# Kernel tuning notes

Measured on AMD Instinct MI355X. Metric: run time of the kernel, lower is better.

Reference implementation:

```python
import jax, jax.numpy as jnp
import numpy as np

N, E = 100_000, 1_600_000
NDIM_IN, EDIM, F, H, C = 64, 32, 32, 3, 10  # F=ndim_out per head, H=num_heads


def _edge_softmax(scores, dst, n):
    # softmax over incoming edges grouped by destination node (DGL edge_softmax)
    m = jax.ops.segment_max(scores, dst, num_segments=n)          # [N,H]
    ex = jnp.exp(scores - m[dst])                                  # [E,H]
    s = jax.ops.segment_sum(ex, dst, num_segments=n)               # [N,H]
    return ex / s[dst]


def _egat_conv(nf, ef, src, dst, W, We, al, ar, ae, b, n):
    # DGL EdgeGATConv: edge features modulate attention logits only
    h, f = al.shape
    ft = (nf @ W).reshape(-1, h, f)      # [N,H,F]
    fe = (ef @ We).reshape(-1, h, f)     # [E,H,F]
    el = (ft * al).sum(-1)               # [N,H]
    er = (ft * ar).sum(-1)               # [N,H]
    ee = (fe * ae).sum(-1)               # [E,H]
    e = jax.nn.leaky_relu(el[src] + er[dst] + ee, 0.2)             # [E,H]
    a = _edge_softmax(e, dst, n)                                   # [E,H]
    rst = jax.ops.segment_sum(ft[src] * a[:, :, None], dst, num_segments=n)
    return rst + b.reshape(1, h, f)


def setup_inputs() -> dict:
    key = jax.random.key(0)
    ks = jax.random.split(key, 16)
    s = lambda k, shp, fan: (jax.random.normal(k, shp, jnp.float32) / np.sqrt(fan).astype(np.float32))
    d = {}
    d["nfeats"] = jax.random.normal(ks[0], (N, 1, NDIM_IN), jnp.float32)
    d["efeats"] = jax.random.normal(ks[1], (E, 1, EDIM), jnp.float32)
    d["src"] = jax.random.randint(ks[2], (E,), 0, N, jnp.int32)
    d["dst"] = jax.random.randint(ks[3], (E,), 0, N, jnp.int32)
    # conv1 params
    d["W1"] = s(ks[4], (NDIM_IN, H * F), NDIM_IN)
    d["We1"] = s(ks[5], (EDIM, H * F), EDIM)
    d["al1"] = s(ks[6], (H, F), F)
    d["ar1"] = s(ks[7], (H, F), F)
    d["ae1"] = s(ks[8], (H, F), F)
    d["b1"] = jnp.zeros((H * F,), jnp.float32)
    # conv2 params (input dim = H*F after head concat)
    d["W2"] = s(ks[9], (H * F, H * F), H * F)
    d["We2"] = s(ks[10], (EDIM, H * F), EDIM)
    d["al2"] = s(ks[11], (H, F), F)
    d["ar2"] = s(ks[12], (H, F), F)
    d["ae2"] = s(ks[13], (H, F), F)
    d["b2"] = jnp.zeros((H * F,), jnp.float32)
    # edge score head: Linear(2*H*F, C)
    d["Wp"] = s(ks[14], (2 * H * F, C), 2 * H * F)
    d["bp"] = jnp.zeros((C,), jnp.float32)
    return d


def reference(nfeats, efeats, src, dst,
              W1, We1, al1, ar1, ae1, b1,
              W2, We2, al2, ar2, ae2, b2,
              Wp, bp):
    n = nfeats.shape[0]
    nf = jnp.squeeze(nfeats, 1)
    ef = jnp.squeeze(efeats, 1)
    h = _egat_conv(nf, ef, src, dst, W1, We1, al1, ar1, ae1, b1, n)
    h = jax.nn.relu(h.reshape(n, -1))                      # [N, H*F]
    h = _egat_conv(h, ef, src, dst, W2, We2, al2, ar2, ae2, b2, n).reshape(n, -1)
    # MLPPredictor: per-edge cat(h_src, h_dst) -> Linear
    score = jnp.concatenate([h[src], h[dst]], axis=1) @ Wp + bp   # [E, C]
    return score
```

## Files before the change

kernel.cpp:

```cpp
#include <hip/hip_runtime.h>
#include <hip/hip_bf16.h>
#include <stdint.h>

typedef __hip_bfloat16 bf16;

__device__ __forceinline__ float b2f(bf16 x) { return __bfloat162float(x); }
__device__ __forceinline__ float bits2f(uint32_t u) {
    union { uint32_t i; float f; } c; c.i = u; return c.f;
}

__global__ void detect_mode_kernel(const uint16_t* __restrict__ nf, int* __restrict__ flag) {
    if (threadIdx.x != 0 || blockIdx.x != 0) return;
    int sane = 0;
    for (int i = 0; i < 256; ++i) {
        uint32_t u = nf[2 * i];
        float a = fabsf(bits2f(u << 16));
        if (a == 0.f || (a > 1e-5f && a < 100.f)) ++sane;
    }
    flag[0] = (sane >= 128) ? 0 : 1;
}

struct ParamTable {
    const void* src[14];
    int off[15];
};

__global__ void convert_params_kernel(ParamTable T, const int* __restrict__ mode,
                                      float* __restrict__ out) {
    int i = blockIdx.x * blockDim.x + threadIdx.x;
    if (i >= T.off[14]) return;
    int k = 0;
    while (k < 13 && i >= T.off[k + 1]) ++k;
    int j = i - T.off[k];
    out[i] = (*mode == 0) ? b2f(((const bf16*)T.src[k])[j]) : ((const float*)T.src[k])[j];
}

__global__ void fold_wae_kernel(const float* __restrict__ We, const float* __restrict__ ae,
                                float* __restrict__ wae) {
    int t = threadIdx.x;
    if (t >= 96) return;
    int d = t / 3, h = t - d * 3;
    float acc = 0.f;
    for (int f = 0; f < 32; ++f) acc += We[d * 96 + h * 32 + f] * ae[h * 32 + f];
    wae[t] = acc;
}

__global__ void hist_kernel(const int* __restrict__ dst, int* __restrict__ cnt, int E) {
    int e = blockIdx.x * blockDim.x + threadIdx.x;
    if (e < E) atomicAdd(&cnt[dst[e]], 1);
}

__global__ void block_sum_kernel(const int* __restrict__ deg, int* __restrict__ bsums, int N) {
    __shared__ int sd[256];
    int t = threadIdx.x;
    int i = blockIdx.x * 256 + t;
    sd[t] = (i < N) ? deg[i] : 0;
    __syncthreads();
    for (int o = 128; o > 0; o >>= 1) {
        if (t < o) sd[t] += sd[t + o];
        __syncthreads();
    }
    if (t == 0) bsums[blockIdx.x] = sd[0];
}

__global__ void scan_bsums_kernel(int* __restrict__ bsums, int nb) {
    __shared__ int a[512], b[512];
    int t = threadIdx.x;
    int v = (t < nb) ? bsums[t] : 0;
    a[t] = v;
    __syncthreads();
    int* in = a;
    int* out = b;
    for (int o = 1; o < 512; o <<= 1) {
        out[t] = in[t] + ((t >= o) ? in[t - o] : 0);
        __syncthreads();
        int* tmp = in; in = out; out = tmp;
    }
    if (t < nb) bsums[t] = in[t] - v;
}

__global__ void scan_expand_kernel(const int* __restrict__ deg, const int* __restrict__ boffs,
                                   int* __restrict__ row_start, int N) {
    __shared__ int a[256], b[256];
    int t = threadIdx.x;
    int i = blockIdx.x * 256 + t;
    int v = (i < N) ? deg[i] : 0;
    a[t] = v;
    __syncthreads();
    int* in = a;
    int* out = b;
    for (int o = 1; o < 256; o <<= 1) {
        out[t] = in[t] + ((t >= o) ? in[t - o] : 0);
        __syncthreads();
        int* tmp = in; in = out; out = tmp;
    }
    if (i < N) row_start[i] = boffs[blockIdx.x] + in[t] - v;
}

__global__ void set_val_kernel(int* __restrict__ p, int v) { p[0] = v; }

__global__ void ft_elr_kernel(const void* __restrict__ X, int kind, const int* __restrict__ mode,
                              int din, const float* __restrict__ W,
                              const float* __restrict__ al, const float* __restrict__ ar,
                              float* __restrict__ ft, float* __restrict__ elr, int N) {
    __shared__ float xs[8 * 96];
    __shared__ float fs[8 * 96];
    int base = blockIdx.x * 8;
    int t = threadIdx.x;
    int m = *mode;
    for (int i = t; i < 8 * din; i += 256) {
        int ln = i / din, d = i - ln * din;
        int node = base + ln;
        float v = 0.f;
        if (node < N) {
            size_t idx = (size_t)node * din + d;
            if (kind == 1)   v = ((const float*)X)[idx];
            else if (m == 0) v = b2f(((const bf16*)X)[idx]);
            else             v = ((const float*)X)[idx];
        }
        xs[ln * 96 + d] = v;
    }
    __syncthreads();
    for (int i = t; i < 768; i += 256) {
        int ln = i / 96, c = i - ln * 96;
        int node = base + ln;
        float acc = 0.f;
        const float* xr = xs + ln * 96;
        for (int d = 0; d < din; ++d) acc += xr[d] * W[d * 96 + c];
        fs[ln * 96 + c] = acc;
        if (node < N) ft[(size_t)node * 96 + c] = acc;
    }
    __syncthreads();
    if (t < 48) {
        int ln = t / 6, q = t - ln * 6;
        int h = q >> 1, isr = q & 1;
        int node = base + ln;
        if (node < N) {
            const float* av = isr ? ar : al;
            const float* fr = fs + ln * 96 + h * 32;
            float acc = 0.f;
            for (int f = 0; f < 32; ++f) acc += fr[f] * av[h * 32 + f];
            elr[node * 6 + isr * 3 + h] = acc;
        }
    }
}

__global__ void scatter_edge_kernel(const void* __restrict__ ef, const int* __restrict__ mode,
                                    const float* __restrict__ wae1, const float* __restrict__ wae2,
                                    const int* __restrict__ src, const int* __restrict__ dst,
                                    const float* __restrict__ elr,
                                    const int* __restrict__ row_start, int* __restrict__ cur,
                                    float4* __restrict__ S, int E) {
    __shared__ float w1[96];
    __shared__ float w2[96];
    int t = threadIdx.x;
    if (t < 96) { w1[t] = wae1[t]; w2[t] = wae2[t]; }
    __syncthreads();
    int e = blockIdx.x * blockDim.x + t;
    if (e >= E) return;
    int m = *mode;

    float x[32];
    if (m == 0) {
        const uint4* p = (const uint4*)((const uint16_t*)ef + (size_t)e * 32);
#pragma unroll
        for (int q = 0; q < 4; ++q) {
            uint4 u = p[q];
            x[q * 8 + 0] = bits2f(u.x << 16); x[q * 8 + 1] = bits2f(u.x & 0xffff0000u);
            x[q * 8 + 2] = bits2f(u.y << 16); x[q * 8 + 3] = bits2f(u.y & 0xffff0000u);
            x[q * 8 + 4] = bits2f(u.z << 16); x[q * 8 + 5] = bits2f(u.z & 0xffff0000u);
            x[q * 8 + 6] = bits2f(u.w << 16); x[q * 8 + 7] = bits2f(u.w & 0xffff0000u);
        }
    } else {
        const float4* p = (const float4*)((const float*)ef + (size_t)e * 32);
#pragma unroll
        for (int q = 0; q < 8; ++q) {
            float4 u = p[q];
            x[q * 4 + 0] = u.x; x[q * 4 + 1] = u.y; x[q * 4 + 2] = u.z; x[q * 4 + 3] = u.w;
        }
    }
    float a0 = 0.f, a1 = 0.f, a2 = 0.f;
    float c0 = 0.f, c1 = 0.f, c2 = 0.f;
#pragma unroll
    for (int d = 0; d < 32; ++d) {
        float xv = x[d];
        a0 += xv * w1[d * 3 + 0];
        a1 += xv * w1[d * 3 + 1];
        a2 += xv * w1[d * 3 + 2];
        c0 += xv * w2[d * 3 + 0];
        c1 += xv * w2[d * 3 + 1];
        c2 += xv * w2[d * 3 + 2];
    }
    int si = src[e], di = dst[e];
    float2 el01 = *(const float2*)(elr + si * 6);
    float  el2  = elr[si * 6 + 2];
    float2 er01 = *(const float2*)(elr + di * 6 + 3);
    float er0 = elr[di * 6 + 3], er1 = elr[di * 6 + 4], er2 = elr[di * 6 + 5];
    (void)er01;
    float l0 = el01.x + er0 + a0;
    float l1 = el01.y + er1 + a1;
    float l2 = el2    + er2 + a2;
    l0 = (l0 > 0.f) ? l0 : 0.2f * l0;
    l1 = (l1 > 0.f) ? l1 : 0.2f * l1;
    l2 = (l2 > 0.f) ? l2 : 0.2f * l2;
    int p = atomicAdd(&cur[di], 1);
    int pos = row_start[di] + p;
    S[2 * pos]     = make_float4(__int_as_float(si), __expf(l0), __expf(l1), __expf(l2));
    S[2 * pos + 1] = make_float4(c0, c1, c2, 0.f);
}

__global__ void aggregate_direct_kernel(const float* __restrict__ ft, const float4* __restrict__ S,
                                        const int* __restrict__ row_start,
                                        const float* __restrict__ bias, int do_relu,
                                        float* __restrict__ R, int N) {
    int t = threadIdx.x;
    int node = blockIdx.x * 8 + (t >> 5);
    int lane = t & 31;
    if (node >= N) return;
    int beg = row_start[node], end = row_start[node + 1];
    float a0 = 0.f, a1 = 0.f, a2 = 0.f, s0 = 0.f, s1 = 0.f, s2 = 0.f;
    int i = beg;
    for (; i + 4 <= end; i += 4) {
        float4 q0 = S[2 * (i + 0)];
        float4 q1 = S[2 * (i + 1)];
        float4 q2 = S[2 * (i + 2)];
        float4 q3 = S[2 * (i + 3)];
        int v0 = __float_as_int(q0.x), v1 = __float_as_int(q1.x);
        int v2 = __float_as_int(q2.x), v3 = __float_as_int(q3.x);
        const float* f0 = ft + (size_t)v0 * 96;
        const float* f1 = ft + (size_t)v1 * 96;
        const float* f2 = ft + (size_t)v2 * 96;
        const float* f3 = ft + (size_t)v3 * 96;
        a0 += f0[lane] * q0.y + f1[lane] * q1.y + f2[lane] * q2.y + f3[lane] * q3.y;
        a1 += f0[lane + 32] * q0.z + f1[lane + 32] * q1.z + f2[lane + 32] * q2.z + f3[lane + 32] * q3.z;
        a2 += f0[lane + 64] * q0.w + f1[lane + 64] * q1.w + f2[lane + 64] * q2.w + f3[lane + 64] * q3.w;
        s0 += q0.y + q1.y + q2.y + q3.y;
        s1 += q0.z + q1.z + q2.z + q3.z;
        s2 += q0.w + q1.w + q2.w + q3.w;
    }
    for (; i < end; ++i) {
        float4 q = S[2 * i];
        int sv = __float_as_int(q.x);
        const float* fr = ft + (size_t)sv * 96;
        a0 += fr[lane] * q.y;
        a1 += fr[lane + 32] * q.z;
        a2 += fr[lane + 64] * q.w;
        s0 += q.y; s1 += q.z; s2 += q.w;
    }
    float r0, r1, r2;
    if (end > beg) { r0 = a0 / s0; r1 = a1 / s1; r2 = a2 / s2; }
    else           { r0 = r1 = r2 = 0.f; }
    r0 += bias[lane]; r1 += bias[lane + 32]; r2 += bias[lane + 64];
    if (do_relu) { r0 = fmaxf(r0, 0.f); r1 = fmaxf(r1, 0.f); r2 = fmaxf(r2, 0.f); }
    float* out = R + (size_t)node * 96;
    out[lane] = r0; out[lane + 32] = r1; out[lane + 64] = r2;
}

__global__ void aggregate_fused_kernel(const float* __restrict__ ft, const float4* __restrict__ S,
                                       const int* __restrict__ row_start,
                                       const float* __restrict__ elr,
                                       const float* __restrict__ bias,
                                       float* __restrict__ R, int N) {
    int t = threadIdx.x;
    int node = blockIdx.x * 8 + (t >> 5);
    int lane = t & 31;
    if (node >= N) return;
    int beg = row_start[node], end = row_start[node + 1];
    float er0 = elr[node * 6 + 3], er1 = elr[node * 6 + 4], er2 = elr[node * 6 + 5];
    float a0 = 0.f, a1 = 0.f, a2 = 0.f, s0 = 0.f, s1 = 0.f, s2 = 0.f;
    int i = beg;
    for (; i + 4 <= end; i += 4) {
#pragma unroll
        for (int u = 0; u < 4; ++u) {
            float4 qa = S[2 * (i + u)];
            float4 qb = S[2 * (i + u) + 1];
            int sv = __float_as_int(qa.x);
            float2 el01 = *(const float2*)(elr + sv * 6);
            float  el2  = elr[sv * 6 + 2];
            float l0 = el01.x + er0 + qb.x;
            float l1 = el01.y + er1 + qb.y;
            float l2 = el2    + er2 + qb.z;
            l0 = (l0 > 0.f) ? l0 : 0.2f * l0;
            l1 = (l1 > 0.f) ? l1 : 0.2f * l1;
            l2 = (l2 > 0.f) ? l2 : 0.2f * l2;
            float e0 = __expf(l0), e1 = __expf(l1), e2 = __expf(l2);
            const float* fr = ft + (size_t)sv * 96;
            a0 += fr[lane] * e0;
            a1 += fr[lane + 32] * e1;
            a2 += fr[lane + 64] * e2;
            s0 += e0; s1 += e1; s2 += e2;
        }
    }
    for (; i < end; ++i) {
        float4 qa = S[2 * i];
        float4 qb = S[2 * i + 1];
        int sv = __float_as_int(qa.x);
        float2 el01 = *(const float2*)(elr + sv * 6);
        float  el2  = elr[sv * 6 + 2];
        float l0 = el01.x + er0 + qb.x;
        float l1 = el01.y + er1 + qb.y;
        float l2 = el2    + er2 + qb.z;
        l0 = (l0 > 0.f) ? l0 : 0.2f * l0;
        l1 = (l1 > 0.f) ? l1 : 0.2f * l1;
        l2 = (l2 > 0.f) ? l2 : 0.2f * l2;
        float e0 = __expf(l0), e1 = __expf(l1), e2 = __expf(l2);
        const float* fr = ft + (size_t)sv * 96;
        a0 += fr[lane] * e0;
        a1 += fr[lane + 32] * e1;
        a2 += fr[lane + 64] * e2;
        s0 += e0; s1 += e1; s2 += e2;
    }
    float r0, r1, r2;
    if (end > beg) { r0 = a0 / s0; r1 = a1 / s1; r2 = a2 / s2; }
    else           { r0 = r1 = r2 = 0.f; }
    r0 += bias[lane]; r1 += bias[lane + 32]; r2 += bias[lane + 64];
    float* out = R + (size_t)node * 96;
    out[lane] = r0; out[lane + 32] = r1; out[lane + 64] = r2;
}

__global__ void uv_kernel(const float* __restrict__ h, const float* __restrict__ Wp,
                          const float* __restrict__ bp, float* __restrict__ uv, int N) {
    __shared__ float hs[8 * 96];
    int base = blockIdx.x * 8;
    int t = threadIdx.x;
    for (int i = t; i < 768; i += 256) {
        int ln = i / 96, c = i - ln * 96;
        int node = base + ln;
        hs[i] = (node < N) ? h[(size_t)node * 96 + c] : 0.f;
    }
    __syncthreads();
    if (t < 160) {
        int ln = t / 20, q = t - ln * 20;
        int half = q / 10, c = q - half * 10;
        int node = base + ln;
        if (node < N) {
            float acc = half ? 0.f : bp[c];
            const float* hr = hs + ln * 96;
            const float* wcol = Wp + half * 960 + c;
            for (int j = 0; j < 96; ++j) acc += hr[j] * wcol[j * 10];
            uv[node * 20 + q] = acc;
        }
    }
}

__global__ void score_kernel(const float* __restrict__ uv, const int* __restrict__ src,
                             const int* __restrict__ dst, const int* __restrict__ mode,
                             void* __restrict__ out, int E) {
    int e = blockIdx.x * blockDim.x + threadIdx.x;
    if (e >= E) return;
    int si = src[e], di = dst[e];
    const float* u = uv + (size_t)si * 20;
    const float* v = uv + (size_t)di * 20 + 10;
    float r[10];
#pragma unroll
    for (int c = 0; c < 10; ++c) r[c] = u[c] + v[c];
    if (*mode == 0) {
        bf16 o[10];
#pragma unroll
        for (int c = 0; c < 10; ++c) o[c] = __float2bfloat16(r[c]);
        uint32_t* po = (uint32_t*)((bf16*)out + (size_t)e * 10);
        const uint32_t* ps = (const uint32_t*)o;
#pragma unroll
        for (int q = 0; q < 5; ++q) po[q] = ps[q];
    } else {
        float2* po = (float2*)((float*)out + (size_t)e * 10);
#pragma unroll
        for (int q = 0; q < 5; ++q) po[q] = make_float2(r[2 * q], r[2 * q + 1]);
    }
}

extern "C" void kernel_launch(void* const* d_in, const int* in_sizes, int n_in,
                              void* d_out, int out_size, void* d_ws, size_t ws_size,
                              hipStream_t stream) {
    const void* nfeats = d_in[0];
    const void* efeats = d_in[1];
    const int* src = (const int*)d_in[2];
    const int* dst = (const int*)d_in[3];

    const int N = in_sizes[0] / 64;
    const int E = in_sizes[2];

    char* w = (char*)d_ws;
    auto alloc = [&](size_t bytes) {
        void* p = (void*)w;
        w += (bytes + 255) & ~(size_t)255;
        return p;
    };
    int*    flag      = (int*)alloc(256);
    float*  pbuf      = (float*)alloc((size_t)24202 * 4);
    float*  wae1      = (float*)alloc(96 * 4);
    float*  wae2      = (float*)alloc(96 * 4);
    float*  R         = (float*)alloc((size_t)N * 96 * 4);
    float*  F         = (float*)alloc((size_t)N * 96 * 4);
    float4* S         = (float4*)alloc((size_t)E * 32);
    float*  elr       = (float*)alloc((size_t)N * 6 * 4);
    int*    row_start = (int*)alloc((size_t)(N + 1) * 4);
    int*    cnt       = (int*)alloc((size_t)N * 4);
    int*    bsums     = (int*)alloc(512 * 4);
    float*  uv        = (float*)S;

    const int ns[14] = {64*96, 32*96, 96, 96, 96, 96, 96*96, 32*96, 96, 96, 96, 96, 192*10, 10};
    ParamTable T;
    int off = 0;
    for (int k = 0; k < 14; ++k) { T.src[k] = d_in[4 + k]; T.off[k] = off; off += ns[k]; }
    T.off[14] = off;
    float* W1f  = pbuf + T.off[0];
    float* We1f = pbuf + T.off[1];
    float* al1f = pbuf + T.off[2];
    float* ar1f = pbuf + T.off[3];
    float* ae1f = pbuf + T.off[4];
    float* b1f  = pbuf + T.off[5];
    float* W2f  = pbuf + T.off[6];
    float* We2f = pbuf + T.off[7];
    float* al2f = pbuf + T.off[8];
    float* ar2f = pbuf + T.off[9];
    float* ae2f = pbuf + T.off[10];
    float* b2f_ = pbuf + T.off[11];
    float* Wpf  = pbuf + T.off[12];
    float* bpf  = pbuf + T.off[13];

    dim3 b256(256);
    int eblocks    = (E + 255) / 256;
    int nodeBlocks = (N + 7) / 8;
    int nb         = (N + 255) / 256;

    hipLaunchKernelGGL(detect_mode_kernel, dim3(1), dim3(64), 0, stream,
                       (const uint16_t*)nfeats, flag);
    hipLaunchKernelGGL(convert_params_kernel, dim3((off + 255) / 256), b256, 0, stream,
                       T, flag, pbuf);
    hipLaunchKernelGGL(fold_wae_kernel, dim3(1), dim3(128), 0, stream, We1f, ae1f, wae1);
    hipLaunchKernelGGL(fold_wae_kernel, dim3(1), dim3(128), 0, stream, We2f, ae2f, wae2);

    hipMemsetAsync(cnt, 0, (size_t)N * 4, stream);
    hipLaunchKernelGGL(hist_kernel, dim3(eblocks), b256, 0, stream, dst, cnt, E);
    hipLaunchKernelGGL(block_sum_kernel, dim3(nb), b256, 0, stream, cnt, bsums, N);
    hipLaunchKernelGGL(scan_bsums_kernel, dim3(1), dim3(512), 0, stream, bsums, nb);
    hipLaunchKernelGGL(scan_expand_kernel, dim3(nb), b256, 0, stream, cnt, bsums, row_start, N);
    hipLaunchKernelGGL(set_val_kernel, dim3(1), dim3(1), 0, stream, row_start + N, E);

    hipLaunchKernelGGL(ft_elr_kernel, dim3(nodeBlocks), b256, 0, stream,
                       nfeats, 0, flag, 64, W1f, al1f, ar1f, F, elr, N);

    hipMemsetAsync(cnt, 0, (size_t)N * 4, stream);
    hipLaunchKernelGGL(scatter_edge_kernel, dim3(eblocks), b256, 0, stream,
                       efeats, flag, wae1, wae2, src, dst, elr, row_start, cnt, S, E);

    hipLaunchKernelGGL(aggregate_direct_kernel, dim3(nodeBlocks), b256, 0, stream,
                       F, S, row_start, b1f, 1, R, N);

    hipLaunchKernelGGL(ft_elr_kernel, dim3(nodeBlocks), b256, 0, stream,
                       (const void*)R, 1, flag, 96, W2f, al2f, ar2f, F, elr, N);
    hipLaunchKernelGGL(aggregate_fused_kernel, dim3(nodeBlocks), b256, 0, stream,
                       F, S, row_start, elr, b2f_, R, N);

    hipLaunchKernelGGL(uv_kernel, dim3(nodeBlocks), b256, 0, stream, R, Wpf, bpf, uv, N);
    hipLaunchKernelGGL(score_kernel, dim3(eblocks), b256, 0, stream,
                       uv, src, dst, flag, d_out, E);
}
```

Before: 1.099 ms.

## Record CSR rank in histogram and defer layer-1 attention to aggregation

The histogram pass now stores each edge's atomic rank, so the scatter pass can place edges without a second memset and a second atomic pass. The scatter no longer needs layer-1 node logits, so it runs before the first node transform and stores raw edge logit terms. Layer-1 attention (leaky-relu, exp) moves into a unified aggregation kernel, the same path layer 2 already used. The cost is an extra E-sized rank buffer plus per-edge gathers of elr and exp work inside aggregation.

After: 1.092 ms. About the same (-0.7%).

```diff
diff --git a/kernel.cpp b/kernel.cpp
--- a/kernel.cpp
+++ b/kernel.cpp
@@ -45,9 +45,10 @@
     wae[t] = acc;
 }
 
-__global__ void hist_kernel(const int* __restrict__ dst, int* __restrict__ cnt, int E) {
+__global__ void hist_rank_kernel(const int* __restrict__ dst, int* __restrict__ cnt,
+                                 int* __restrict__ rank, int E) {
     int e = blockIdx.x * blockDim.x + threadIdx.x;
-    if (e < E) atomicAdd(&cnt[dst[e]], 1);
+    if (e < E) rank[e] = atomicAdd(&cnt[dst[e]], 1);
 }
 
 __global__ void block_sum_kernel(const int* __restrict__ deg, int* __restrict__ bsums, int N) {
@@ -148,8 +149,8 @@
 __global__ void scatter_edge_kernel(const void* __restrict__ ef, const int* __restrict__ mode,
                                     const float* __restrict__ wae1, const float* __restrict__ wae2,
                                     const int* __restrict__ src, const int* __restrict__ dst,
-                                    const float* __restrict__ elr,
-                                    const int* __restrict__ row_start, int* __restrict__ cur,
+                                    const int* __restrict__ rank,
+                                    const int* __restrict__ row_start,
                                     float4* __restrict__ S, int E) {
     __shared__ float w1[96];
     __shared__ float w2[96];
@@ -192,75 +193,17 @@
         c2 += xv * w2[d * 3 + 2];
     }
     int si = src[e], di = dst[e];
-    float2 el01 = *(const float2*)(elr + si * 6);
-    float  el2  = elr[si * 6 + 2];
-    float2 er01 = *(const float2*)(elr + di * 6 + 3);
-    float er0 = elr[di * 6 + 3], er1 = elr[di * 6 + 4], er2 = elr[di * 6 + 5];
-    (void)er01;
-    float l0 = el01.x + er0 + a0;
-    float l1 = el01.y + er1 + a1;
-    float l2 = el2    + er2 + a2;
-    l0 = (l0 > 0.f) ? l0 : 0.2f * l0;
-    l1 = (l1 > 0.f) ? l1 : 0.2f * l1;
-    l2 = (l2 > 0.f) ? l2 : 0.2f * l2;
-    int p = atomicAdd(&cur[di], 1);
-    int pos = row_start[di] + p;
-    S[2 * pos]     = make_float4(__int_as_float(si), __expf(l0), __expf(l1), __expf(l2));
+    int pos = row_start[di] + rank[e];
+    S[2 * pos]     = make_float4(__int_as_float(si), a0, a1, a2);
     S[2 * pos + 1] = make_float4(c0, c1, c2, 0.f);
 }
 
-__global__ void aggregate_direct_kernel(const float* __restrict__ ft, const float4* __restrict__ S,
-                                        const int* __restrict__ row_start,
-                                        const float* __restrict__ bias, int do_relu,
-                                        float* __restrict__ R, int N) {
-    int t = threadIdx.x;
-    int node = blockIdx.x * 8 + (t >> 5);
-    int lane = t & 31;
-    if (node >= N) return;
-    int beg = row_start[node], end = row_start[node + 1];
-    float a0 = 0.f, a1 = 0.f, a2 = 0.f, s0 = 0.f, s1 = 0.f, s2 = 0.f;
-    int i = beg;
-    for (; i + 4 <= end; i += 4) {
-        float4 q0 = S[2 * (i + 0)];
-        float4 q1 = S[2 * (i + 1)];
-        float4 q2 = S[2 * (i + 2)];
-        float4 q3 = S[2 * (i + 3)];
-        int v0 = __float_as_int(q0.x), v1 = __float_as_int(q1.x);
-        int v2 = __float_as_int(q2.x), v3 = __float_as_int(q3.x);
-        const float* f0 = ft + (size_t)v0 * 96;
-        const float* f1 = ft + (size_t)v1 * 96;
-        const float* f2 = ft + (size_t)v2 * 96;
-        const float* f3 = ft + (size_t)v3 * 96;
-        a0 += f0[lane] * q0.y + f1[lane] * q1.y + f2[lane] * q2.y + f3[lane] * q3.y;
-        a1 += f0[lane + 32] * q0.z + f1[lane + 32] * q1.z + f2[lane + 32] * q2.z + f3[lane + 32] * q3.z;
-        a2 += f0[lane + 64] * q0.w + f1[lane + 64] * q1.w + f2[lane + 64] * q2.w + f3[lane + 64] * q3.w;
-        s0 += q0.y + q1.y + q2.y + q3.y;
-        s1 += q0.z + q1.z + q2.z + q3.z;
-        s2 += q0.w + q1.w + q2.w + q3.w;
-    }
-    for (; i < end; ++i) {
-        float4 q = S[2 * i];
-        int sv = __float_as_int(q.x);
-        const float* fr = ft + (size_t)sv * 96;
-        a0 += fr[lane] * q.y;
-        a1 += fr[lane + 32] * q.z;
-        a2 += fr[lane + 64] * q.w;
-        s0 += q.y; s1 += q.z; s2 += q.w;
-    }
-    float r0, r1, r2;
-    if (end > beg) { r0 = a0 / s0; r1 = a1 / s1; r2 = a2 / s2; }
-    else           { r0 = r1 = r2 = 0.f; }
-    r0 += bias[lane]; r1 += bias[lane + 32]; r2 += bias[lane + 64];
-    if (do_relu) { r0 = fmaxf(r0, 0.f); r1 = fmaxf(r1, 0.f); r2 = fmaxf(r2, 0.f); }
-    float* out = R + (size_t)node * 96;
-    out[lane] = r0; out[lane + 32] = r1; out[lane + 64] = r2;
-}
-
-__global__ void aggregate_fused_kernel(const float* __restrict__ ft, const float4* __restrict__ S,
-                                       const int* __restrict__ row_start,
-                                       const float* __restrict__ elr,
-                                       const float* __restrict__ bias,
-                                       float* __restrict__ R, int N) {
+__global__ void aggregate_kernel(const float* __restrict__ ft, const float4* __restrict__ S,
+                                 const int* __restrict__ row_start,
+                                 const float* __restrict__ elr,
+                                 const float* __restrict__ bias,
+                                 int use_qa, int do_relu,
+                                 float* __restrict__ R, int N) {
     int t = threadIdx.x;
     int node = blockIdx.x * 8 + (t >> 5);
     int lane = t & 31;
@@ -275,11 +218,14 @@
             float4 qa = S[2 * (i + u)];
             float4 qb = S[2 * (i + u) + 1];
             int sv = __float_as_int(qa.x);
+            float ee0, ee1, ee2;
+            if (use_qa) { ee0 = qa.y; ee1 = qa.z; ee2 = qa.w; }
+            else        { ee0 = qb.x; ee1 = qb.y; ee2 = qb.z; }
             float2 el01 = *(const float2*)(elr + sv * 6);
             float  el2  = elr[sv * 6 + 2];
-            float l0 = el01.x + er0 + qb.x;
-            float l1 = el01.y + er1 + qb.y;
-            float l2 = el2    + er2 + qb.z;
+            float l0 = el01.x + er0 + ee0;
+            float l1 = el01.y + er1 + ee1;
+            float l2 = el2    + er2 + ee2;
             l0 = (l0 > 0.f) ? l0 : 0.2f * l0;
             l1 = (l1 > 0.f) ? l1 : 0.2f * l1;
             l2 = (l2 > 0.f) ? l2 : 0.2f * l2;
@@ -295,11 +241,14 @@
         float4 qa = S[2 * i];
         float4 qb = S[2 * i + 1];
         int sv = __float_as_int(qa.x);
+        float ee0, ee1, ee2;
+        if (use_qa) { ee0 = qa.y; ee1 = qa.z; ee2 = qa.w; }
+        else        { ee0 = qb.x; ee1 = qb.y; ee2 = qb.z; }
         float2 el01 = *(const float2*)(elr + sv * 6);
         float  el2  = elr[sv * 6 + 2];
-        float l0 = el01.x + er0 + qb.x;
-        float l1 = el01.y + er1 + qb.y;
-        float l2 = el2    + er2 + qb.z;
+        float l0 = el01.x + er0 + ee0;
+        float l1 = el01.y + er1 + ee1;
+        float l2 = el2    + er2 + ee2;
         l0 = (l0 > 0.f) ? l0 : 0.2f * l0;
         l1 = (l1 > 0.f) ? l1 : 0.2f * l1;
         l2 = (l2 > 0.f) ? l2 : 0.2f * l2;
@@ -314,6 +263,7 @@
     if (end > beg) { r0 = a0 / s0; r1 = a1 / s1; r2 = a2 / s2; }
     else           { r0 = r1 = r2 = 0.f; }
     r0 += bias[lane]; r1 += bias[lane + 32]; r2 += bias[lane + 64];
+    if (do_relu) { r0 = fmaxf(r0, 0.f); r1 = fmaxf(r1, 0.f); r2 = fmaxf(r2, 0.f); }
     float* out = R + (size_t)node * 96;
     out[lane] = r0; out[lane + 32] = r1; out[lane + 64] = r2;
 }
@@ -397,6 +347,7 @@
     int*    row_start = (int*)alloc((size_t)(N + 1) * 4);
     int*    cnt       = (int*)alloc((size_t)N * 4);
     int*    bsums     = (int*)alloc(512 * 4);
+    int*    rank      = (int*)alloc((size_t)E * 4);
     float*  uv        = (float*)S;
 
     const int ns[14] = {64*96, 32*96, 96, 96, 96, 96, 96*96, 32*96, 96, 96, 96, 96, 192*10, 10};
@@ -432,26 +383,24 @@
     hipLaunchKernelGGL(fold_wae_kernel, dim3(1), dim3(128), 0, stream, We2f, ae2f, wae2);
 
     hipMemsetAsync(cnt, 0, (size_t)N * 4, stream);
-    hipLaunchKernelGGL(hist_kernel, dim3(eblocks), b256, 0, stream, dst, cnt, E);
+    hipLaunchKernelGGL(hist_rank_kernel, dim3(eblocks), b256, 0, stream, dst, cnt, rank, E);
     hipLaunchKernelGGL(block_sum_kernel, dim3(nb), b256, 0, stream, cnt, bsums, N);
     hipLaunchKernelGGL(scan_bsums_kernel, dim3(1), dim3(512), 0, stream, bsums, nb);
     hipLaunchKernelGGL(scan_expand_kernel, dim3(nb), b256, 0, stream, cnt, bsums, row_start, N);
     hipLaunchKernelGGL(set_val_kernel, dim3(1), dim3(1), 0, stream, row_start + N, E);
 
+    hipLaunchKernelGGL(scatter_edge_kernel, dim3(eblocks), b256, 0, stream,
+                       efeats, flag, wae1, wae2, src, dst, rank, row_start, S, E);
+
     hipLaunchKernelGGL(ft_elr_kernel, dim3(nodeBlocks), b256, 0, stream,
                        nfeats, 0, flag, 64, W1f, al1f, ar1f, F, elr, N);
-
-    hipMemsetAsync(cnt, 0, (size_t)N * 4, stream);
-    hipLaunchKernelGGL(scatter_edge_kernel, dim3(eblocks), b256, 0, stream,
-                       efeats, flag, wae1, wae2, src, dst, elr, row_start, cnt, S, E);
-
-    hipLaunchKernelGGL(aggregate_direct_kernel, dim3(nodeBlocks), b256, 0, stream,
-                       F, S, row_start, b1f, 1, R, N);
+    hipLaunchKernelGGL(aggregate_kernel, dim3(nodeBlocks), b256, 0, stream,
+                       F, S, row_start, elr, b1f, 1, 1, R, N);
 
     hipLaunchKernelGGL(ft_elr_kernel, dim3(nodeBlocks), b256, 0, stream,
                        (const void*)R, 1, flag, 96, W2f, al2f, ar2f, F, elr, N);
-    hipLaunchKernelGGL(aggregate_fused_kernel, dim3(nodeBlocks), b256, 0, stream,
-                       F, S, row_start, elr, b2f_, R, N);
+    hipLaunchKernelGGL(aggregate_kernel, dim3(nodeBlocks), b256, 0, stream,
+                       F, S, row_start, elr, b2f_, 0, 0, R, N);
 
     hipLaunchKernelGGL(uv_kernel, dim3(nodeBlocks), b256, 0, stream, R, Wpf, bpf, uv, N);
     hipLaunchKernelGGL(score_kernel, dim3(eblocks), b256, 0, stream,
```
